# Performance work log

Measured on AMD Instinct MI355X. Metric: run time of the kernel, lower is better.

The kernel has to match this reference:

```python
import jax, jax.numpy as jnp
import numpy as np

H = 256
B, S = 32, 1024

def setup_inputs() -> dict:
    key = jax.random.key(0)
    ks = jax.random.split(key, 7)
    scale = 1.0 / np.sqrt(H)
    return {
        "x": jax.random.normal(ks[0], (B, S, H), dtype=jnp.float32),
        "Wq": jax.random.uniform(ks[1], (H, H), jnp.float32, -scale, scale),
        "bq": jax.random.uniform(ks[2], (H,), jnp.float32, -scale, scale),
        "Wk": jax.random.uniform(ks[3], (H, H), jnp.float32, -scale, scale),
        "bk": jax.random.uniform(ks[4], (H,), jnp.float32, -scale, scale),
        "Wv": jax.random.uniform(ks[5], (H, H), jnp.float32, -scale, scale),
        "bv": jax.random.uniform(ks[6], (H,), jnp.float32, -scale, scale),
    }

def reference(x, Wq, bq, Wk, bk, Wv, bv):
    # torch Linear: y = x @ W^T + b
    q = jnp.einsum('bsh,oh->bso', x, Wq) + bq  # [B,S,H]
    k = jnp.einsum('bsh,oh->bso', x, Wk) + bk
    v = jnp.einsum('bsh,oh->bso', x, Wv) + bv
    scores = jnp.einsum('bqh,bkh->bqk', q, k) / jnp.sqrt(jnp.float32(q.shape[-1]))
    # Faithful to original: softmax over dim=1 (the QUERY axis), not the key axis.
    attn = jax.nn.softmax(scores, axis=1)  # [B,S,S]
    context = jnp.einsum('bqk,bkh->bqh', attn, v)  # [B,S,H]
    return jnp.sum(context, axis=1)  # [B,H]
```

## Files before the change

### kernel.cpp

```cpp
#include <hip/hip_runtime.h>

#define BB 32
#define SS 1024
#define HH 256
#define SPLITS 16
#define ROWS_PER_BLOCK (SS / SPLITS)


__global__ __launch_bounds__(256) void xsum_partial_kernel(
    const float* __restrict__ x, float* __restrict__ partials) {
    const int blk   = blockIdx.x;
    const int b     = blk / SPLITS;
    const int split = blk % SPLITS;
    const int tid   = threadIdx.x;
    const int h4    = tid & 63;
    const int srow  = tid >> 6;

    const float4* xb = reinterpret_cast<const float4*>(
        x + (size_t)b * SS * HH + (size_t)split * ROWS_PER_BLOCK * HH);

    float4 acc = make_float4(0.f, 0.f, 0.f, 0.f);
    #pragma unroll 4
    for (int r = srow; r < ROWS_PER_BLOCK; r += 4) {
        float4 v = xb[(size_t)r * (HH / 4) + h4];
        acc.x += v.x; acc.y += v.y; acc.z += v.z; acc.w += v.w;
    }

    __shared__ float4 lds[256];
    lds[tid] = acc;
    __syncthreads();
    if (tid < 64) {
        float4 a0 = lds[tid];
        float4 a1 = lds[tid + 64];
        float4 a2 = lds[tid + 128];
        float4 a3 = lds[tid + 192];
        float4 r;
        r.x = (a0.x + a1.x) + (a2.x + a3.x);
        r.y = (a0.y + a1.y) + (a2.y + a3.y);
        r.z = (a0.z + a1.z) + (a2.z + a3.z);
        r.w = (a0.w + a1.w) + (a2.w + a3.w);
        reinterpret_cast<float4*>(
            partials + ((size_t)b * SPLITS + split) * HH)[h4] = r;
    }
}

__global__ __launch_bounds__(256) void out_kernel(
    const float* __restrict__ partials, const float* __restrict__ Wv,
    const float* __restrict__ bv, float* __restrict__ out) {
    const int b = blockIdx.x;
    const int h = threadIdx.x;

    __shared__ float xsum[HH];
    float s = 0.f;
    #pragma unroll
    for (int c = 0; c < SPLITS; ++c)
        s += partials[((size_t)b * SPLITS + c) * HH + h];
    xsum[h] = s;
    __syncthreads();

    const float4* wrow = reinterpret_cast<const float4*>(Wv + (size_t)h * HH);
    const float4* xs   = reinterpret_cast<const float4*>(xsum);
    float acc = (float)SS * bv[h];
    #pragma unroll 8
    for (int i = 0; i < HH / 4; ++i) {
        float4 w  = wrow[i];
        float4 xv = xs[i];
        acc += w.x * xv.x + w.y * xv.y + w.z * xv.z + w.w * xv.w;
    }
    out[(size_t)b * HH + h] = acc;
}

extern "C" void kernel_launch(void* const* d_in, const int* in_sizes, int n_in,
                              void* d_out, int out_size, void* d_ws, size_t ws_size,
                              hipStream_t stream) {
    const float* x  = (const float*)d_in[0];
    const float* Wv = (const float*)d_in[5];
    const float* bv = (const float*)d_in[6];
    float* out = (float*)d_out;
    float* partials = (float*)d_ws;

    xsum_partial_kernel<<<BB * SPLITS, 256, 0, stream>>>(x, partials);
    out_kernel<<<BB, 256, 0, stream>>>(partials, Wv, bv, out);
}
```

Before: 19.25 us.

## Fuse x-sum reduction and Wv projection into one kernel with atomic accumulation

```diff
diff --git a/kernel.cpp b/kernel.cpp
--- a/kernel.cpp
+++ b/kernel.cpp
@@ -4,29 +4,31 @@
 #define SS 1024
 #define HH 256
 #define SPLITS 16
-#define ROWS_PER_BLOCK (SS / SPLITS)
+#define ROWS (SS / SPLITS)
 
 
-__global__ __launch_bounds__(256) void xsum_partial_kernel(
-    const float* __restrict__ x, float* __restrict__ partials) {
+__global__ __launch_bounds__(256) void fused_atomic_kernel(
+    const float* __restrict__ x, const float* __restrict__ Wv,
+    const float* __restrict__ bv, float* __restrict__ out) {
     const int blk   = blockIdx.x;
-    const int b     = blk / SPLITS;
-    const int split = blk % SPLITS;
+    const int b     = blk >> 4;
+    const int split = blk & 15;
     const int tid   = threadIdx.x;
     const int h4    = tid & 63;
-    const int srow  = tid >> 6;
+    const int ph    = tid >> 6;
 
     const float4* xb = reinterpret_cast<const float4*>(
-        x + (size_t)b * SS * HH + (size_t)split * ROWS_PER_BLOCK * HH);
+        x + (size_t)b * SS * HH + (size_t)split * ROWS * HH);
 
     float4 acc = make_float4(0.f, 0.f, 0.f, 0.f);
-    #pragma unroll 4
-    for (int r = srow; r < ROWS_PER_BLOCK; r += 4) {
+    #pragma unroll
+    for (int r = ph; r < ROWS; r += 4) {
         float4 v = xb[(size_t)r * (HH / 4) + h4];
         acc.x += v.x; acc.y += v.y; acc.z += v.z; acc.w += v.w;
     }
 
     __shared__ float4 lds[256];
+    __shared__ float xsum[HH];
     lds[tid] = acc;
     __syncthreads();
     if (tid < 64) {
@@ -39,35 +41,21 @@
         r.y = (a0.y + a1.y) + (a2.y + a3.y);
         r.z = (a0.z + a1.z) + (a2.z + a3.z);
         r.w = (a0.w + a1.w) + (a2.w + a3.w);
-        reinterpret_cast<float4*>(
-            partials + ((size_t)b * SPLITS + split) * HH)[h4] = r;
+        reinterpret_cast<float4*>(xsum)[tid] = r;
     }
-}
-
-__global__ __launch_bounds__(256) void out_kernel(
-    const float* __restrict__ partials, const float* __restrict__ Wv,
-    const float* __restrict__ bv, float* __restrict__ out) {
-    const int b = blockIdx.x;
-    const int h = threadIdx.x;
-
-    __shared__ float xsum[HH];
-    float s = 0.f;
-    #pragma unroll
-    for (int c = 0; c < SPLITS; ++c)
-        s += partials[((size_t)b * SPLITS + c) * HH + h];
-    xsum[h] = s;
     __syncthreads();
 
+    const int h = tid;
     const float4* wrow = reinterpret_cast<const float4*>(Wv + (size_t)h * HH);
     const float4* xs   = reinterpret_cast<const float4*>(xsum);
-    float acc = (float)SS * bv[h];
+    float o = (split == 0) ? (float)SS * bv[h] : 0.f;
     #pragma unroll 8
     for (int i = 0; i < HH / 4; ++i) {
         float4 w  = wrow[i];
         float4 xv = xs[i];
-        acc += w.x * xv.x + w.y * xv.y + w.z * xv.z + w.w * xv.w;
+        o += w.x * xv.x + w.y * xv.y + w.z * xv.z + w.w * xv.w;
     }
-    out[(size_t)b * HH + h] = acc;
+    atomicAdd(&out[(size_t)b * HH + h], o);
 }
 
 extern "C" void kernel_launch(void* const* d_in, const int* in_sizes, int n_in,
@@ -77,8 +65,8 @@
     const float* Wv = (const float*)d_in[5];
     const float* bv = (const float*)d_in[6];
     float* out = (float*)d_out;
-    float* partials = (float*)d_ws;
 
-    xsum_partial_kernel<<<BB * SPLITS, 256, 0, stream>>>(x, partials);
-    out_kernel<<<BB, 256, 0, stream>>>(partials, Wv, bv, out);
+    hipMemsetAsync(out, 0, (size_t)BB * HH * sizeof(float), stream);
+
+    fused_atomic_kernel<<<BB * SPLITS, 256, 0, stream>>>(x, Wv, bv, out);
 }
```

Result: slower. 30.10 us (+56.4%).
